# Kernel tuning notes

Measured on AMD Instinct MI355X. Metric: run time of the kernel, lower is better.

Reference implementation:

```python
import jax, jax.numpy as jnp
from jax import lax
import numpy as np

B, C, H, W = 8, 192, 128, 128
HEADS, WS, SS = 6, 8, 4
HID = 768  # 4 * C
HEAD_DIM = C // HEADS
SCALE = HEAD_DIM ** -0.5
EPS = 1e-5


def _rel_pos_index(ws):
    coords = np.stack(np.meshgrid(np.arange(ws), np.arange(ws), indexing='ij'))  # (2, ws, ws)
    flat = coords.reshape(2, ws * ws)
    rel = flat[:, :, None] - flat[:, None, :]          # (2, N, N)
    rel = rel.transpose(1, 2, 0)                       # (N, N, 2)
    rel[:, :, 0] += ws - 1
    rel[:, :, 1] += ws - 1
    rel[:, :, 0] *= 2 * ws - 1
    return rel.sum(-1).astype(np.int32)                # (N, N)


def _attn_mask(hp, wp, ws, ss):
    # Swin shift mask: 0 where tokens share a region, -100 otherwise. (nW, N, N)
    img = np.zeros((hp, wp), dtype=np.float32)
    slices = (slice(0, -ws), slice(-ws, -ss), slice(-ss, None))
    cnt = 0
    for hs in slices:
        for ws_ in slices:
            img[hs, ws_] = float(cnt)
            cnt += 1
    mw = img.reshape(hp // ws, ws, wp // ws, ws).transpose(0, 2, 1, 3).reshape(-1, ws * ws)
    am = mw[:, None, :] - mw[:, :, None]
    return np.where(am != 0, -100.0, 0.0).astype(np.float32)


def _layernorm(x, g, b):
    mu = jnp.mean(x, axis=-1, keepdims=True)
    var = jnp.mean(jnp.square(x - mu), axis=-1, keepdims=True)
    return (x - mu) * lax.rsqrt(var + EPS) * g + b


def setup_inputs() -> dict:
    key = jax.random.key(0)
    ks = jax.random.split(key, 16)
    s = 0.02
    return {
        'x': jax.random.normal(ks[0], (B, C, H, W), jnp.float32),
        'pos_conv_w': jax.random.normal(ks[1], (C, 1, 3, 3), jnp.float32) * s,
        'norm1_g': jnp.ones((C,), jnp.float32),
        'norm1_b': jnp.zeros((C,), jnp.float32),
        'qkv_w': jax.random.normal(ks[2], (C, 3 * C), jnp.float32) * s,
        'qkv_b': jnp.zeros((3 * C,), jnp.float32),
        'proj_w': jax.random.normal(ks[3], (C, C), jnp.float32) * s,
        'proj_b': jnp.zeros((C,), jnp.float32),
        'rel_bias_table': jax.random.normal(ks[4], ((2 * WS - 1) ** 2, HEADS), jnp.float32) * s,
        'norm2_g': jnp.ones((C,), jnp.float32),
        'norm2_b': jnp.zeros((C,), jnp.float32),
        'mlp_w1': jax.random.normal(ks[5], (C, HID), jnp.float32) * s,
        'mlp_b1': jnp.zeros((HID,), jnp.float32),
        'mlp_w2': jax.random.normal(ks[6], (HID, C), jnp.float32) * s,
        'mlp_b2': jnp.zeros((C,), jnp.float32),
    }


def reference(x, pos_conv_w, norm1_g, norm1_b, qkv_w, qkv_b, proj_w, proj_b,
              rel_bias_table, norm2_g, norm2_b, mlp_w1, mlp_b1, mlp_w2, mlp_b2):
    b, c, h, w = x.shape
    ws, ss, nh, hd = WS, SS, HEADS, HEAD_DIM
    N = ws * ws

    # depthwise 3x3 positional conv (residual)
    x = x + lax.conv_general_dilated(
        x, pos_conv_w, (1, 1), 'SAME', feature_group_count=c,
        dimension_numbers=('NCHW', 'OIHW', 'NCHW'))

    if ss > 0:
        x = jnp.roll(x, (-ss, -ss), axis=(2, 3))

    pad_h = (ws - h % ws) % ws
    pad_w = (ws - w % ws) % ws
    if pad_h or pad_w:
        x = jnp.pad(x, ((0, 0), (0, 0), (0, pad_h), (0, pad_w)))
    hp, wp = h + pad_h, w + pad_w

    # window partition -> (num_windows, N, c)
    windows = x.reshape(b, c, hp // ws, ws, wp // ws, ws)
    windows = windows.transpose(0, 2, 4, 3, 5, 1).reshape(-1, N, c)
    nw = windows.shape[0]

    a = _layernorm(windows, norm1_g, norm1_b)
    qkv = (a @ qkv_w + qkv_b).reshape(nw, N, 3, nh, hd).transpose(2, 0, 3, 1, 4)
    q, k, v = qkv[0], qkv[1], qkv[2]                      # (nw, nh, N, hd)

    attn = jnp.einsum('whnd,whmd->whnm', q * SCALE, k)    # (nw, nh, N, N)

    rel_idx = jnp.asarray(_rel_pos_index(ws))             # (N, N) int
    bias = rel_bias_table[rel_idx.reshape(-1)].reshape(N, N, nh).transpose(2, 0, 1)
    attn = attn + bias[None]

    if ss > 0:
        mask = jnp.asarray(_attn_mask(hp, wp, ws, ss))    # (nW_per_img, N, N)
        nwpb = (hp // ws) * (wp // ws)
        attn = attn.reshape(b, nwpb, nh, N, N) + mask[None, :, None]
        attn = attn.reshape(nw, nh, N, N)

    attn = jax.nn.softmax(attn, axis=-1)
    out = jnp.einsum('whnm,whmd->whnd', attn, v).transpose(0, 2, 1, 3).reshape(nw, N, c)

    windows = windows + out @ proj_w + proj_b
    hmid = jax.nn.gelu(_layernorm(windows, norm2_g, norm2_b) @ mlp_w1 + mlp_b1, approximate=False)
    windows = windows + hmid @ mlp_w2 + mlp_b2

    # unpartition -> (b, c, hp, wp), crop, roll back
    y = windows.reshape(b, hp // ws, wp // ws, ws, ws, c)
    y = y.transpose(0, 5, 1, 3, 2, 4).reshape(b, c, hp, wp)[:, :, :h, :w]
    if ss > 0:
        y = jnp.roll(y, (ss, ss), axis=(2, 3))
    return y
```

## Files before the change

### kernel.cpp

```cpp
#include <hip/hip_runtime.h>
#include <hip/hip_bf16.h>
#include <cstdint>
#include <cstddef>

typedef short short8 __attribute__((ext_vector_type(8)));
typedef float float4_ __attribute__((ext_vector_type(4)));
typedef unsigned int uint4_ __attribute__((ext_vector_type(4)));
typedef unsigned int uint2_ __attribute__((ext_vector_type(2)));

#define DEVI static __device__ __forceinline__

DEVI unsigned short f2bf(float f) {
  union { float f; unsigned u; } v; v.f = f;
  return (unsigned short)((v.u + 0x7FFFu + ((v.u >> 16) & 1u)) >> 16);
}
DEVI unsigned pack2bf(float a, float b) {
  return (unsigned)f2bf(a) | ((unsigned)f2bf(b) << 16);
}
DEVI unsigned short f2bfc(float f) {
  __hip_bfloat16 h = __float2bfloat16(f);
  union { __hip_bfloat16 h1; unsigned short u; } cv; cv.h1 = h; return cv.u;
}
DEVI unsigned pack2bfc(float a, float b) {
  float2 f2; f2.x = a; f2.y = b;
  __hip_bfloat162 h = __float22bfloat162_rn(f2);
  union { __hip_bfloat162 h2; unsigned u; } cv; cv.h2 = h; return cv.u;
}
DEVI float bf2f(unsigned short h) {
  union { unsigned u; float f; } v; v.u = ((unsigned)h) << 16;
  return v.f;
}
DEVI float gelu_f(float x) {
  float u = x * (0.7978845608f + 0.0356774081f * x * x);
  float e = exp2f(-2.8853900818f * u);
  return x * __builtin_amdgcn_rcpf(1.0f + e);
}

#define SCALE_Q 0.17677669529663687f

__global__ __launch_bounds__(256) void k_prep(
    const float* __restrict__ qkv_w, const float* __restrict__ qkv_b,
    const float* __restrict__ proj_w, const float* __restrict__ mlp_w1,
    const float* __restrict__ mlp_w2, const float* __restrict__ relt,
    unsigned short* __restrict__ qkvWT, unsigned short* __restrict__ projWT,
    unsigned short* __restrict__ w1T, unsigned short* __restrict__ w2T,
    float* __restrict__ qkv_b_s, float* __restrict__ bias_attn) {
  int i = blockIdx.x * 256 + threadIdx.x;
  if (i < 110592) { int n = i / 192, k = i - n * 192;
    float v = qkv_w[k * 576 + n]; if (n < 192) v *= SCALE_Q;
    qkvWT[i] = f2bf(v); return; }
  i -= 110592;
  if (i < 576) { qkv_b_s[i] = qkv_b[i] * (i < 192 ? SCALE_Q : 1.0f); return; }
  i -= 576;
  if (i < 36864) { int n = i / 192, k = i - n * 192;
    projWT[i] = f2bf(proj_w[k * 192 + n]); return; }
  i -= 36864;
  if (i < 147456) { int n = i / 192, k = i - n * 192;
    w1T[i] = f2bf(mlp_w1[k * 768 + n]); return; }
  i -= 147456;
  if (i < 147456) { int n = i / 768, k = i - n * 768;
    w2T[i] = f2bf(mlp_w2[k * 192 + n]); return; }
  i -= 147456;
  if (i < 24576) {
    int h = i >> 12, nm = i & 4095, n = nm >> 6, m = nm & 63;
    int dr = (n >> 3) - (m >> 3) + 7, dc = (n & 7) - (m & 7) + 7;
    bias_attn[i] = relt[(dr * 15 + dc) * 6 + h];
  }
}

__global__ __launch_bounds__(256) void k_conv(
    const float* __restrict__ x, const float* __restrict__ convw,
    unsigned short* __restrict__ temp) {
  __shared__ float s_in[66 * 128];
  int bx = blockIdx.x;
  int c = bx >> 1, seg = bx & 1, b = blockIdx.y;
  int h0 = seg * 64;
  int t = threadIdx.x;
  const float* xp = x + ((size_t)(b * 192 + c)) * 16384;
  #pragma unroll
  for (int i = 0; i < 9; ++i) {
    int q = t + i * 256;
    if (q < 2112) {
      int srow = q >> 5, chunk = q & 31;
      float4_ v = *(const float4_*)(xp + ((h0 + 3 + srow) & 127) * 128 + chunk * 4);
      *(float4_*)(s_in + srow * 128 + chunk * 4) = v;
    }
  }
  float cw9[9];
  #pragma unroll
  for (int i = 0; i < 9; ++i) cw9[i] = convw[c * 9 + i];
  __syncthreads();
  int r2 = t >> 7;
  int wp = t & 127;
  int w_true = (wp + 4) & 127;
  float mw0 = (w_true != 0) ? 1.f : 0.f;
  float mw2 = (w_true != 127) ? 1.f : 0.f;
  int wl0 = (w_true + 127) & 127, wl2 = (w_true + 1) & 127;
  unsigned short* tp = temp + ((size_t)(b * 192 + c)) * 16384;
  #pragma unroll 4
  for (int it = 0; it < 32; ++it) {
    int r = it * 2 + r2;
    int h_true = (h0 + 4 + r) & 127;
    float mh0 = (h_true != 0) ? 1.f : 0.f;
    float mh2 = (h_true != 127) ? 1.f : 0.f;
    const float* row0 = s_in + r * 128;
    const float* row1 = row0 + 128;
    const float* row2 = row1 + 128;
    float acc = row1[w_true];
    acc = fmaf(cw9[0], mh0 * mw0 * row0[wl0], acc);
    acc = fmaf(cw9[1], mh0 * row0[w_true], acc);
    acc = fmaf(cw9[2], mh0 * mw2 * row0[wl2], acc);
    acc = fmaf(cw9[3], mw0 * row1[wl0], acc);
    acc = fmaf(cw9[4], row1[w_true], acc);
    acc = fmaf(cw9[5], mw2 * row1[wl2], acc);
    acc = fmaf(cw9[6], mh2 * mw0 * row2[wl0], acc);
    acc = fmaf(cw9[7], mh2 * row2[w_true], acc);
    acc = fmaf(cw9[8], mh2 * mw2 * row2[wl2], acc);
    tp[(size_t)(h0 + r) * 128 + wp] = f2bf(acc);
  }
}

__global__ __launch_bounds__(256) void k_lnw(
    const unsigned short* __restrict__ temp, const float* __restrict__ g1,
    const float* __restrict__ b1, unsigned short* __restrict__ xw,
    unsigned short* __restrict__ a) {
  __shared__ unsigned short sT[192 * 128];
  __shared__ float s_g[192], s_b[192];
  int t = threadIdx.x;
  for (int i = t; i < 192; i += 256) { s_g[i] = g1[i]; s_b[i] = b1[i]; }
  int wj0 = blockIdx.x * 2, wi = blockIdx.y, b = blockIdx.z;
  const unsigned short* tb = temp + (size_t)b * (192 * 16384) + (wi * 8) * 128 + wj0 * 8;
  #pragma unroll
  for (int i = 0; i < 12; ++i) {
    int id = t + i * 256;
    int c = id >> 4, rem = id & 15, r = rem >> 1, piece = rem & 1;
    short8 v = *(const short8*)(tb + (size_t)c * 16384 + r * 128 + piece * 8);
    *(short8*)(sT + c * 128 + piece * 64 + r * 8) = v;
  }
  __syncthreads();
  int tok = t >> 1, half = t & 1, c0 = half * 96;
  size_t gtok = ((size_t)(b * 256 + wi * 16 + wj0 + (tok >> 6))) * 64 + (tok & 63);
  unsigned short* xwp = xw + gtok * 192 + c0;
  float sum = 0.f, sq = 0.f;
  #pragma unroll
  for (int j8 = 0; j8 < 12; ++j8) {
    unsigned short raw[8];
    unsigned pk[4];
    #pragma unroll
    for (int e = 0; e < 8; ++e) {
      unsigned short rv = sT[(c0 + j8 * 8 + e) * 128 + tok];
      raw[e] = rv;
      float x = bf2f(rv);
      sum += x; sq = fmaf(x, x, sq);
    }
    #pragma unroll
    for (int k = 0; k < 4; ++k) pk[k] = (unsigned)raw[2 * k] | ((unsigned)raw[2 * k + 1] << 16);
    uint4_ pv = { pk[0], pk[1], pk[2], pk[3] };
    *(uint4_*)(xwp + j8 * 8) = pv;
  }
  sum += __shfl_xor(sum, 1);
  sq  += __shfl_xor(sq, 1);
  float mu = sum * (1.f / 192.f);
  float var = sq * (1.f / 192.f) - mu * mu;
  float rs = rsqrtf(var + 1e-5f);
  unsigned short* ap = a + gtok * 192 + c0;
  #pragma unroll
  for (int j8 = 0; j8 < 12; ++j8) {
    unsigned pk[4];
    #pragma unroll
    for (int k = 0; k < 4; ++k) {
      int c = c0 + j8 * 8 + k * 2;
      float v0 = (bf2f(sT[c * 128 + tok]) - mu) * rs * s_g[c] + s_b[c];
      float v1 = (bf2f(sT[(c + 1) * 128 + tok]) - mu) * rs * s_g[c + 1] + s_b[c + 1];
      pk[k] = pack2bf(v0, v1);
    }
    uint4_ pv = { pk[0], pk[1], pk[2], pk[3] };
    *(uint4_*)(ap + j8 * 8) = pv;
  }
}

__global__ __launch_bounds__(64, 2) void k_qkvattn(
    const unsigned short* __restrict__ a, const unsigned short* __restrict__ wT,
    const float* __restrict__ qbias, const float* __restrict__ biasAll,
    unsigned short* __restrict__ outO) {
  __shared__ __align__(16) unsigned short sQK[4096];
  __shared__ __align__(16) unsigned short sVT[2048];
  int lane = threadIdx.x;
  int head = blockIdx.y;
  int win = blockIdx.x;
  int wi = (win >> 4) & 15, wj = win & 15;
  int lrow = lane & 15, lkgrp = lane >> 4, lk = lkgrp * 8;
  const unsigned short* aWin = a + (size_t)win * (64 * 192);
  const unsigned short* wbase = wT + (size_t)head * 32 * 192;
  char* qk = (char*)sQK;
  char* vt = (char*)sVT;

  float4_ acc[3][2][4];
  #pragma unroll
  for (int s = 0; s < 3; ++s)
    #pragma unroll
    for (int nb = 0; nb < 2; ++nb)
      #pragma unroll
      for (int mi = 0; mi < 4; ++mi) acc[s][nb][mi] = (float4_){0.f, 0.f, 0.f, 0.f};
  short8 bwA[6], bwB[6], af0[4], af1[4];
  #pragma unroll
  for (int s = 0; s < 3; ++s)
    #pragma unroll
    for (int nb = 0; nb < 2; ++nb)
      bwA[s * 2 + nb] = *(const short8*)(wbase + (size_t)(s * 192 + nb * 16 + lrow) * 192 + lk);
  #pragma unroll
  for (int mi = 0; mi < 4; ++mi)
    af0[mi] = *(const short8*)(aWin + (size_t)(mi * 16 + lrow) * 192 + lk);
  #pragma unroll
  for (int s = 0; s < 3; ++s)
    #pragma unroll
    for (int nb = 0; nb < 2; ++nb)
      bwB[s * 2 + nb] = *(const short8*)(wbase + (size_t)(s * 192 + nb * 16 + lrow) * 192 + 32 + lk);
  #pragma unroll
  for (int mi = 0; mi < 4; ++mi)
    af1[mi] = *(const short8*)(aWin + (size_t)(mi * 16 + lrow) * 192 + 32 + lk);
  #pragma unroll
  for (int ks = 0; ks < 6; ++ks) {
    #pragma unroll
    for (int mi = 0; mi < 4; ++mi) {
      short8 a_ = (ks & 1) ? af1[mi] : af0[mi];
      #pragma unroll
      for (int sn = 0; sn < 6; ++sn) {
        short8 b_ = (ks & 1) ? bwB[sn] : bwA[sn];
        acc[sn >> 1][sn & 1][mi] =
            __builtin_amdgcn_mfma_f32_16x16x32_bf16(b_, a_, acc[sn >> 1][sn & 1][mi], 0, 0, 0);
      }
    }
    if (ks < 4) {
      int kc = (ks + 2) * 32 + lk;
      #pragma unroll
      for (int s = 0; s < 3; ++s)
        #pragma unroll
        for (int nb = 0; nb < 2; ++nb) {
          short8 nv = *(const short8*)(wbase + (size_t)(s * 192 + nb * 16 + lrow) * 192 + kc);
          if (ks & 1) bwB[s * 2 + nb] = nv; else bwA[s * 2 + nb] = nv;
        }
      #pragma unroll
      for (int mi = 0; mi < 4; ++mi) {
        short8 nv = *(const short8*)(aWin + (size_t)(mi * 16 + lrow) * 192 + kc);
        if (ks & 1) af1[mi] = nv; else af0[mi] = nv;
      }
    }
  }
  #pragma unroll
  for (int sel = 0; sel < 2; ++sel) {
    #pragma unroll
    for (int nb = 0; nb < 2; ++nb) {
      float4_ b4 = *(const float4_*)(qbias + sel * 192 + head * 32 + nb * 16 + lkgrp * 4);
      int dsub2 = (nb * 16 + lkgrp * 4) * 2;
      #pragma unroll
      for (int mi = 0; mi < 4; ++mi) {
        int tok = mi * 16 + lrow;
        uint2_ pv = { pack2bfc(acc[sel][nb][mi][0] + b4[0], acc[sel][nb][mi][1] + b4[1]),
                      pack2bfc(acc[sel][nb][mi][2] + b4[2], acc[sel][nb][mi][3] + b4[3]) };
        *(uint2_*)(qk + sel * 4096 + ((tok * 64 + dsub2) ^ ((tok & 7) << 4))) = pv;
      }
    }
  }
  #pragma unroll
  for (int nb = 0; nb < 2; ++nb) {
    float4_ b4 = *(const float4_*)(qbias + 384 + head * 32 + nb * 16 + lkgrp * 4);
    #pragma unroll
    for (int mi = 0; mi < 4; ++mi) {
      int tok = mi * 16 + lrow;
      #pragma unroll
      for (int e = 0; e < 4; ++e) {
        int d = nb * 16 + lkgrp * 4 + e;
        *(unsigned short*)(vt + ((d * 128 + tok * 2) ^ ((d & 7) << 4))) =
            f2bfc(acc[2][nb][mi][e] + b4[e]);
      }
    }
  }

  short8 kf[4];
  #pragma unroll
  for (int ni = 0; ni < 4; ++ni) {
    int tokk = ni * 16 + lrow;
    kf[ni] = *(const short8*)(qk + 4096 + ((tokk * 64 + lk * 2) ^ ((tokk & 7) << 4)));
  }
  float4_ s[4][4];
  __builtin_amdgcn_s_setprio(1);
  #pragma unroll
  for (int mi = 0; mi < 4; ++mi) {
    int tokq = mi * 16 + lrow;
    short8 qf = *(const short8*)(qk + ((tokq * 64 + lk * 2) ^ ((tokq & 7) << 4)));
    #pragma unroll
    for (int ni = 0; ni < 4; ++ni) {
      s[mi][ni] = (float4_){0.f, 0.f, 0.f, 0.f};
      s[mi][ni] = __builtin_amdgcn_mfma_f32_16x16x32_bf16(qf, kf[ni], s[mi][ni], 0, 0, 0);
    }
  }
  __builtin_amdgcn_s_setprio(0);
  const float* bh = biasAll + head * 4096;
  bool wi15 = (wi == 15), wj15 = (wj == 15);
  bool edge = wi15 || wj15;
  #pragma unroll
  for (int mi = 0; mi < 4; ++mi) {
    #pragma unroll
    for (int e = 0; e < 4; ++e) {
      int row = mi * 16 + lkgrp * 4 + e;
      int rcls = (wi15 ? ((row >> 3) >= 4 ? 2 : 1) : 0) * 3 +
                 (wj15 ? ((row & 7) >= 4 ? 2 : 1) : 0);
      float v[4];
      #pragma unroll
      for (int ni = 0; ni < 4; ++ni) {
        int col = ni * 16 + lrow;
        float xv = s[mi][ni][e] + bh[row * 64 + col];
        if (edge) {
          int ccls = (wi15 ? ((col >> 3) >= 4 ? 2 : 1) : 0) * 3 +
                     (wj15 ? ((col & 7) >= 4 ? 2 : 1) : 0);
          if (ccls != rcls) xv -= 100.f;
        }
        v[ni] = xv;
      }
      float mx = fmaxf(fmaxf(v[0], v[1]), fmaxf(v[2], v[3]));
      mx = fmaxf(mx, __shfl_xor(mx, 1));
      mx = fmaxf(mx, __shfl_xor(mx, 2));
      mx = fmaxf(mx, __shfl_xor(mx, 4));
      mx = fmaxf(mx, __shfl_xor(mx, 8));
      float sm = 0.f;
      #pragma unroll
      for (int ni = 0; ni < 4; ++ni) { v[ni] = __expf(v[ni] - mx); sm += v[ni]; }
      sm += __shfl_xor(sm, 1);
      sm += __shfl_xor(sm, 2);
      sm += __shfl_xor(sm, 4);
      sm += __shfl_xor(sm, 8);
      float inv = 1.f / sm;
      #pragma unroll
      for (int ni = 0; ni < 4; ++ni) {
        int col = ni * 16 + lrow;
        *(unsigned short*)(qk + ((row * 128 + col * 2) ^ ((row & 7) << 4))) = f2bfc(v[ni] * inv);
      }
    }
  }
  float4_ o[2][4];
  #pragma unroll
  for (int db = 0; db < 2; ++db)
    #pragma unroll
    for (int qb2 = 0; qb2 < 4; ++qb2) o[db][qb2] = (float4_){0.f, 0.f, 0.f, 0.f};
  __builtin_amdgcn_s_setprio(1);
  #pragma unroll
  for (int kk = 0; kk < 2; ++kk) {
    int ktok = kk * 32 + lk;
    short8 vf[2], pf[4];
    #pragma unroll
    for (int db = 0; db < 2; ++db) {
      int d = db * 16 + lrow;
      vf[db] = *(const short8*)(vt + ((d * 128 + ktok * 2) ^ ((d & 7) << 4)));
    }
    #pragma unroll
    for (int qb2 = 0; qb2 < 4; ++qb2) {
      int rq = qb2 * 16 + lrow;
      pf[qb2] = *(const short8*)(qk + ((rq * 128 + ktok * 2) ^ ((rq & 7) << 4)));
    }
    #pragma unroll
    for (int db = 0; db < 2; ++db)
      #pragma unroll
      for (int qb2 = 0; qb2 < 4; ++qb2)
        o[db][qb2] = __builtin_amdgcn_mfma_f32_16x16x32_bf16(vf[db], pf[qb2], o[db][qb2], 0, 0, 0);
  }
  __builtin_amdgcn_s_setprio(0);
  unsigned short* ob = outO + (size_t)win * (64 * 192);
  #pragma unroll
  for (int qb2 = 0; qb2 < 4; ++qb2)
    #pragma unroll
    for (int db = 0; db < 2; ++db) {
      unsigned lo = pack2bfc(o[db][qb2][0], o[db][qb2][1]);
      unsigned hi = pack2bfc(o[db][qb2][2], o[db][qb2][3]);
      uint2_ pv = { lo, hi };
      *(uint2_*)(ob + (size_t)(qb2 * 16 + lrow) * 192 + head * 32 + db * 16 + lkgrp * 4) = pv;
    }
}

__global__ __launch_bounds__(256, 2) void k_mlp(
    const unsigned short* __restrict__ O, const unsigned short* __restrict__ xw,
    const unsigned short* __restrict__ projWT, const float* __restrict__ proj_b,
    const float* __restrict__ n2g, const float* __restrict__ n2b,
    const unsigned short* __restrict__ w1T, const float* __restrict__ mlpb1,
    const unsigned short* __restrict__ w2T, const float* __restrict__ mlpb2,
    float* __restrict__ y) {
  __shared__ __align__(16) unsigned short sH[64 * 192];
  __shared__ __align__(16) unsigned short sB2[64 * 192];
  __shared__ float sRed[64 * 8];
  __shared__ unsigned sTok[64];
  int t = threadIdx.x, lane = t & 63, wn = t >> 6;
  int lrow = lane & 15, lkgrp = lane >> 4, lk = lkgrp * 8;
  int blk = blockIdx.x;
  int b = blk >> 8, rem = blk & 255, ta = rem >> 3, tb_ = rem & 7;
  if (t < 64) {
    int rr = t >> 4, ss = t & 15;
    int h = ta * 4 + rr, w = tb_ * 16 + ss;
    int hp = (h + 124) & 127, wp = (w + 124) & 127;
    unsigned gtok = ((unsigned)(b * 256 + (hp >> 3) * 16 + (wp >> 3))) * 64 +
                    (hp & 7) * 8 + (wp & 7);
    sTok[t] = gtok * 192u;
  }
  __syncthreads();
  unsigned aoff[4];
  #pragma unroll
  for (int mi = 0; mi < 4; ++mi) aoff[mi] = sTok[mi * 16 + lrow];
  float4_ tacc[4][3];
  #pragma unroll
  for (int mi = 0; mi < 4; ++mi)
    #pragma unroll
    for (int ni = 0; ni < 3; ++ni) tacc[mi][ni] = (float4_){0.f, 0.f, 0.f, 0.f};
  {
    short8 bP0[3][3], bP1[3][3], af0[4], af1[4];
    #pragma unroll
    for (int ni = 0; ni < 3; ++ni)
      #pragma unroll
      for (int k3 = 0; k3 < 3; ++k3)
        bP0[ni][k3] = *(const short8*)(projWT + (size_t)(wn * 48 + ni * 16 + lrow) * 192 + k3 * 32 + lk);
    #pragma unroll
    for (int mi = 0; mi < 4; ++mi)
      af0[mi] = *(const short8*)(O + aoff[mi] + lk);
    #pragma unroll
    for (int ni = 0; ni < 3; ++ni)
      #pragma unroll
      for (int k3 = 0; k3 < 3; ++k3)
        bP1[ni][k3] = *(const short8*)(projWT + (size_t)(wn * 48 + ni * 16 + lrow) * 192 + (3 + k3) * 32 + lk);
    #pragma unroll
    for (int mi = 0; mi < 4; ++mi)
      af1[mi] = *(const short8*)(O + aoff[mi] + 32 + lk);
    #pragma unroll
    for (int ks = 0; ks < 6; ++ks) {
      #pragma unroll
      for (int mi = 0; mi < 4; ++mi) {
        short8 a_ = (ks & 1) ? af1[mi] : af0[mi];
        #pragma unroll
        for (int ni = 0; ni < 3; ++ni) {
          short8 b_ = (ks < 3) ? bP0[ni][ks] : bP1[ni][ks - 3];
          tacc[mi][ni] = __builtin_amdgcn_mfma_f32_16x16x32_bf16(a_, b_, tacc[mi][ni], 0, 0, 0);
        }
      }
      if (ks < 4) {
        #pragma unroll
        for (int mi = 0; mi < 4; ++mi) {
          short8 nv = *(const short8*)(O + aoff[mi] + (ks + 2) * 32 + lk);
          if (ks & 1) af1[mi] = nv; else af0[mi] = nv;
        }
      }
    }
  }
  {
    unsigned roff[4][4];
    #pragma unroll
    for (int mi = 0; mi < 4; ++mi)
      #pragma unroll
      for (int e = 0; e < 4; ++e)
        roff[mi][e] = sTok[mi * 16 + lkgrp * 4 + e];
    unsigned short rxv[3][4][4];
    #pragma unroll
    for (int ni = 0; ni < 3; ++ni) {
      int col = wn * 48 + ni * 16 + lrow;
      #pragma unroll
      for (int mi = 0; mi < 4; ++mi)
        #pragma unroll
        for (int e = 0; e < 4; ++e)
          rxv[ni][mi][e] = xw[roff[mi][e] + col];
    }
    #pragma unroll
    for (int ni = 0; ni < 3; ++ni) {
      float pbv = proj_b[wn * 48 + ni * 16 + lrow];
      #pragma unroll
      for (int mi = 0; mi < 4; ++mi)
        #pragma unroll
        for (int e = 0; e < 4; ++e)
          tacc[mi][ni][e] += pbv + bf2f(rxv[ni][mi][e]);
    }
  }
  #pragma unroll
  for (int mi = 0; mi < 4; ++mi)
    #pragma unroll
    for (int e = 0; e < 4; ++e) {
      float s1 = tacc[mi][0][e] + tacc[mi][1][e] + tacc[mi][2][e];
      float s2 = tacc[mi][0][e] * tacc[mi][0][e] + tacc[mi][1][e] * tacc[mi][1][e] +
                 tacc[mi][2][e] * tacc[mi][2][e];
      s1 += __shfl_xor(s1, 1); s1 += __shfl_xor(s1, 2); s1 += __shfl_xor(s1, 4); s1 += __shfl_xor(s1, 8);
      s2 += __shfl_xor(s2, 1); s2 += __shfl_xor(s2, 2); s2 += __shfl_xor(s2, 4); s2 += __shfl_xor(s2, 8);
      if (lrow == 0) {
        int row = mi * 16 + lkgrp * 4 + e;
        sRed[row * 8 + wn * 2 + 0] = s1;
        sRed[row * 8 + wn * 2 + 1] = s2;
      }
    }
  __syncthreads();
  #pragma unroll
  for (int mi = 0; mi < 4; ++mi)
    #pragma unroll
    for (int e = 0; e < 4; ++e) {
      int row = mi * 16 + lkgrp * 4 + e;
      float s1 = sRed[row * 8] + sRed[row * 8 + 2] + sRed[row * 8 + 4] + sRed[row * 8 + 6];
      float s2 = sRed[row * 8 + 1] + sRed[row * 8 + 3] + sRed[row * 8 + 5] + sRed[row * 8 + 7];
      float mu = s1 * (1.f / 192.f);
      float var = s2 * (1.f / 192.f) - mu * mu;
      float rs = rsqrtf(var + 1e-5f);
      #pragma unroll
      for (int ni = 0; ni < 3; ++ni) {
        int col = wn * 48 + ni * 16 + lrow;
        float hv = (tacc[mi][ni][e] - mu) * rs * n2g[col] + n2b[col];
        *(unsigned short*)((char*)sH + ((row * 384 + col * 2) ^ ((row & 7) << 4))) = f2bfc(hv);
      }
    }
  __syncthreads();
  short8 bwA[6], bwB[6];
  #pragma unroll
  for (int ks = 0; ks < 6; ++ks)
    bwA[ks] = *(const short8*)(w1T + (size_t)(wn * 48 + lrow) * 192 + ks * 32 + lk);
  #pragma unroll 1
  for (int ch = 0; ch < 4; ++ch) {
    #pragma unroll 1
    for (int ni = 0; ni < 3; ++ni) {
      int nni = (ni < 2) ? ni + 1 : 0;
      int nch = (ni < 2) ? ch : ch + 1;
      if (nch < 4) {
        int gn = nch * 192 + wn * 48 + nni * 16 + lrow;
        #pragma unroll
        for (int ks = 0; ks < 6; ++ks)
          bwB[ks] = *(const short8*)(w1T + (size_t)gn * 192 + ks * 32 + lk);
      }
      float4_ h1[4];
      #pragma unroll
      for (int mi = 0; mi < 4; ++mi) h1[mi] = (float4_){0.f, 0.f, 0.f, 0.f};
      __builtin_amdgcn_s_setprio(1);
      #pragma unroll
      for (int ks = 0; ks < 6; ++ks) {
        int kb = ks * 32 + lk;
        #pragma unroll
        for (int mi = 0; mi < 4; ++mi) {
          int row = mi * 16 + lrow;
          short8 afv = *(const short8*)((const char*)sH + ((row * 384 + kb * 2) ^ ((row & 7) << 4)));
          h1[mi] = __builtin_amdgcn_mfma_f32_16x16x32_bf16(bwA[ks], afv, h1[mi], 0, 0, 0);
        }
      }
      __builtin_amdgcn_s_setprio(0);
      float4_ b4 = *(const float4_*)(mlpb1 + ch * 192 + wn * 48 + ni * 16 + lkgrp * 4);
      int nsub2 = (wn * 48 + ni * 16 + lkgrp * 4) * 2;
      #pragma unroll
      for (int mi = 0; mi < 4; ++mi) {
        int tok_ = mi * 16 + lrow;
        float g0 = gelu_f(h1[mi][0] + b4[0]);
        float g1 = gelu_f(h1[mi][1] + b4[1]);
        float g2 = gelu_f(h1[mi][2] + b4[2]);
        float g3 = gelu_f(h1[mi][3] + b4[3]);
        uint2_ pv = { pack2bfc(g0, g1), pack2bfc(g2, g3) };
        *(uint2_*)((char*)sB2 + ((tok_ * 384 + nsub2) ^ ((tok_ & 7) << 4))) = pv;
      }
      #pragma unroll
      for (int ks = 0; ks < 6; ++ks) bwA[ks] = bwB[ks];
    }
    short8 cw0[3][3], cw1[3][3];
    #pragma unroll
    for (int ni = 0; ni < 3; ++ni)
      #pragma unroll
      for (int k3 = 0; k3 < 3; ++k3)
        cw0[ni][k3] = *(const short8*)(w2T + (size_t)(wn * 48 + ni * 16 + lrow) * 768 + ch * 192 + k3 * 32 + lk);
    __syncthreads();
    #pragma unroll
    for (int ni = 0; ni < 3; ++ni)
      #pragma unroll
      for (int k3 = 0; k3 < 3; ++k3)
        cw1[ni][k3] = *(const short8*)(w2T + (size_t)(wn * 48 + ni * 16 + lrow) * 768 + ch * 192 + (3 + k3) * 32 + lk);
    __builtin_amdgcn_s_setprio(1);
    #pragma unroll
    for (int ks = 0; ks < 6; ++ks) {
      int kb = ks * 32 + lk;
      short8 af[4];
      #pragma unroll
      for (int mi = 0; mi < 4; ++mi) {
        int row = mi * 16 + lrow;
        af[mi] = *(const short8*)((const char*)sB2 + ((row * 384 + kb * 2) ^ ((row & 7) << 4)));
      }
      #pragma unroll
      for (int mi = 0; mi < 4; ++mi)
        #pragma unroll
        for (int ni = 0; ni < 3; ++ni) {
          short8 b_ = (ks < 3) ? cw0[ni][ks] : cw1[ni][ks - 3];
          tacc[mi][ni] = __builtin_amdgcn_mfma_f32_16x16x32_bf16(af[mi], b_, tacc[mi][ni], 0, 0, 0);
        }
    }
    __builtin_amdgcn_s_setprio(0);
    __syncthreads();
  }
  int wcol = tb_ * 16 + lkgrp * 4;
  #pragma unroll
  for (int ni = 0; ni < 3; ++ni) {
    int col = wn * 48 + ni * 16 + lrow;
    float b2v = mlpb2[col];
    #pragma unroll
    for (int mi = 0; mi < 4; ++mi) {
      int h = ta * 4 + mi;
      float4_ vv;
      #pragma unroll
      for (int e = 0; e < 4; ++e) vv[e] = tacc[mi][ni][e] + b2v;
      *(float4_*)(y + ((size_t)(b * 192 + col) * 128 + h) * 128 + wcol) = vv;
    }
  }
}

extern "C" void kernel_launch(void* const* d_in, const int* in_sizes, int n_in,
                              void* d_out, int out_size, void* d_ws, size_t ws_size,
                              hipStream_t stream) {
  (void)in_sizes; (void)n_in; (void)out_size;
  const float* x    = (const float*)d_in[0];
  const float* pcw  = (const float*)d_in[1];
  const float* n1g  = (const float*)d_in[2];
  const float* n1b  = (const float*)d_in[3];
  const float* qkvw = (const float*)d_in[4];
  const float* qkvb = (const float*)d_in[5];
  const float* pw   = (const float*)d_in[6];
  const float* pb   = (const float*)d_in[7];
  const float* relt = (const float*)d_in[8];
  const float* n2g  = (const float*)d_in[9];
  const float* n2b  = (const float*)d_in[10];
  const float* w1   = (const float*)d_in[11];
  const float* mb1  = (const float*)d_in[12];
  const float* w2   = (const float*)d_in[13];
  const float* mb2  = (const float*)d_in[14];
  float* y = (float*)d_out;
  char* ws = (char*)d_ws;
  size_t off = 0;
  auto carve = [&](size_t bytes) { void* p = ws + off; off += (bytes + 255) & ~(size_t)255; return p; };
  unsigned short* qkvWT  = (unsigned short*)carve(576 * 192 * 2);
  unsigned short* projWT = (unsigned short*)carve(192 * 192 * 2);
  unsigned short* w1T    = (unsigned short*)carve(768 * 192 * 2);
  unsigned short* w2T    = (unsigned short*)carve(192 * 768 * 2);
  float* qkv_b_s   = (float*)carve(576 * 4);
  float* bias_attn = (float*)carve(6 * 64 * 64 * 4);
  unsigned short* aBuf   = (unsigned short*)carve((size_t)131072 * 192 * 2);
  unsigned short* xwBuf  = (unsigned short*)carve((size_t)131072 * 192 * 2);
  unsigned short* temp   = (unsigned short*)carve((size_t)131072 * 192 * 2);
  if (off > ws_size) return;

  k_prep<<<dim3(1827), dim3(256), 0, stream>>>(qkvw, qkvb, pw, w1, w2, relt,
                                               qkvWT, projWT, w1T, w2T, qkv_b_s, bias_attn);
  k_conv<<<dim3(384, 8), dim3(256), 0, stream>>>(x, pcw, temp);
  k_lnw<<<dim3(8, 16, 8), dim3(256), 0, stream>>>(temp, n1g, n1b, xwBuf, aBuf);
  k_qkvattn<<<dim3(2048, 6), dim3(64), 0, stream>>>(aBuf, qkvWT, qkv_b_s, bias_attn, temp);
  k_mlp<<<dim3(2048), dim3(256), 0, stream>>>(temp, xwBuf, projWT, pb, n2g, n2b,
                                              w1T, mb1, w2T, mb2, y);
}
```

Measured before the change: 496.7 us.

## Merge attention heads into one block and double-buffer MLP hidden chunks

The QKV+attention kernel now runs one 384-thread block per window, with one wave per head and per-head shared buffers, instead of one 64-thread block per (window, head). This lets the six heads share the window's activation reads through cache and cuts the block count. In the MLP kernel, the first GEMM now computes all three 16-column tiles per chunk at once with k-step weight streaming. The GELU output alternates between two shared buffers so the trailing per-chunk barrier can be dropped, and the next chunk's weights are prefetched during the second GEMM. The cost is more registers for the h1 accumulators, more shared memory, and possibly lower occupancy.

```diff
diff --git a/kernel.cpp b/kernel.cpp
--- a/kernel.cpp
+++ b/kernel.cpp
@@ -179,21 +179,20 @@
   }
 }
 
-__global__ __launch_bounds__(64, 2) void k_qkvattn(
+__global__ __launch_bounds__(384, 1) void k_qkvattn(
     const unsigned short* __restrict__ a, const unsigned short* __restrict__ wT,
     const float* __restrict__ qbias, const float* __restrict__ biasAll,
     unsigned short* __restrict__ outO) {
-  __shared__ __align__(16) unsigned short sQK[4096];
-  __shared__ __align__(16) unsigned short sVT[2048];
-  int lane = threadIdx.x;
-  int head = blockIdx.y;
+  __shared__ __align__(16) unsigned short sQK[6][4096];
+  __shared__ __align__(16) unsigned short sVT[6][2048];
+  int t = threadIdx.x, lane = t & 63, head = t / 64;
   int win = blockIdx.x;
   int wi = (win >> 4) & 15, wj = win & 15;
   int lrow = lane & 15, lkgrp = lane >> 4, lk = lkgrp * 8;
   const unsigned short* aWin = a + (size_t)win * (64 * 192);
   const unsigned short* wbase = wT + (size_t)head * 32 * 192;
-  char* qk = (char*)sQK;
-  char* vt = (char*)sVT;
+  char* qk = (char*)sQK[head];
+  char* vt = (char*)sVT[head];
 
   float4_ acc[3][2][4];
   #pragma unroll
@@ -204,18 +203,14 @@
       for (int mi = 0; mi < 4; ++mi) acc[s][nb][mi] = (float4_){0.f, 0.f, 0.f, 0.f};
   short8 bwA[6], bwB[6], af0[4], af1[4];
   #pragma unroll
-  for (int s = 0; s < 3; ++s)
-    #pragma unroll
-    for (int nb = 0; nb < 2; ++nb)
-      bwA[s * 2 + nb] = *(const short8*)(wbase + (size_t)(s * 192 + nb * 16 + lrow) * 192 + lk);
+  for (int sn = 0; sn < 6; ++sn)
+    bwA[sn] = *(const short8*)(wbase + (size_t)((sn >> 1) * 192 + (sn & 1) * 16 + lrow) * 192 + lk);
   #pragma unroll
   for (int mi = 0; mi < 4; ++mi)
     af0[mi] = *(const short8*)(aWin + (size_t)(mi * 16 + lrow) * 192 + lk);
   #pragma unroll
-  for (int s = 0; s < 3; ++s)
-    #pragma unroll
-    for (int nb = 0; nb < 2; ++nb)
-      bwB[s * 2 + nb] = *(const short8*)(wbase + (size_t)(s * 192 + nb * 16 + lrow) * 192 + 32 + lk);
+  for (int sn = 0; sn < 6; ++sn)
+    bwB[sn] = *(const short8*)(wbase + (size_t)((sn >> 1) * 192 + (sn & 1) * 16 + lrow) * 192 + 32 + lk);
   #pragma unroll
   for (int mi = 0; mi < 4; ++mi)
     af1[mi] = *(const short8*)(aWin + (size_t)(mi * 16 + lrow) * 192 + 32 + lk);
@@ -234,12 +229,10 @@
     if (ks < 4) {
       int kc = (ks + 2) * 32 + lk;
       #pragma unroll
-      for (int s = 0; s < 3; ++s)
-        #pragma unroll
-        for (int nb = 0; nb < 2; ++nb) {
-          short8 nv = *(const short8*)(wbase + (size_t)(s * 192 + nb * 16 + lrow) * 192 + kc);
-          if (ks & 1) bwB[s * 2 + nb] = nv; else bwA[s * 2 + nb] = nv;
-        }
+      for (int sn = 0; sn < 6; ++sn) {
+        short8 nv = *(const short8*)(wbase + (size_t)((sn >> 1) * 192 + (sn & 1) * 16 + lrow) * 192 + kc);
+        if (ks & 1) bwB[sn] = nv; else bwA[sn] = nv;
+      }
       #pragma unroll
       for (int mi = 0; mi < 4; ++mi) {
         short8 nv = *(const short8*)(aWin + (size_t)(mi * 16 + lrow) * 192 + kc);
@@ -385,7 +378,7 @@
     const unsigned short* __restrict__ w2T, const float* __restrict__ mlpb2,
     float* __restrict__ y) {
   __shared__ __align__(16) unsigned short sH[64 * 192];
-  __shared__ __align__(16) unsigned short sB2[64 * 192];
+  __shared__ __align__(16) unsigned short sB2[2][64 * 192];
   __shared__ float sRed[64 * 8];
   __shared__ unsigned sTok[64];
   int t = threadIdx.x, lane = t & 63, wn = t >> 6;
@@ -508,51 +501,59 @@
       }
     }
   __syncthreads();
-  short8 bwA[6], bwB[6];
-  #pragma unroll
-  for (int ks = 0; ks < 6; ++ks)
-    bwA[ks] = *(const short8*)(w1T + (size_t)(wn * 48 + lrow) * 192 + ks * 32 + lk);
+  short8 wA[3], wB[3];
+  #pragma unroll
+  for (int ni = 0; ni < 3; ++ni)
+    wA[ni] = *(const short8*)(w1T + (size_t)(wn * 48 + ni * 16 + lrow) * 192 + lk);
+  #pragma unroll
+  for (int ni = 0; ni < 3; ++ni)
+    wB[ni] = *(const short8*)(w1T + (size_t)(wn * 48 + ni * 16 + lrow) * 192 + 32 + lk);
   #pragma unroll 1
   for (int ch = 0; ch < 4; ++ch) {
-    #pragma unroll 1
+    char* sBc = (char*)sB2[ch & 1];
+    float4_ h1[4][3];
+    #pragma unroll
+    for (int mi = 0; mi < 4; ++mi)
+      #pragma unroll
+      for (int ni = 0; ni < 3; ++ni) h1[mi][ni] = (float4_){0.f, 0.f, 0.f, 0.f};
+    __builtin_amdgcn_s_setprio(1);
+    #pragma unroll
+    for (int ks = 0; ks < 6; ++ks) {
+      int kb = ks * 32 + lk;
+      #pragma unroll
+      for (int mi = 0; mi < 4; ++mi) {
+        int row = mi * 16 + lrow;
+        short8 afv = *(const short8*)((const char*)sH + ((row * 384 + kb * 2) ^ ((row & 7) << 4)));
+        #pragma unroll
+        for (int ni = 0; ni < 3; ++ni) {
+          short8 b_ = (ks & 1) ? wB[ni] : wA[ni];
+          h1[mi][ni] = __builtin_amdgcn_mfma_f32_16x16x32_bf16(b_, afv, h1[mi][ni], 0, 0, 0);
+        }
+      }
+      if (ks < 4) {
+        int kc = (ks + 2) * 32 + lk;
+        #pragma unroll
+        for (int ni = 0; ni < 3; ++ni) {
+          short8 nv = *(const short8*)(w1T + (size_t)(ch * 192 + wn * 48 + ni * 16 + lrow) * 192 + kc);
+          if (ks & 1) wB[ni] = nv; else wA[ni] = nv;
+        }
+      }
+    }
+    __builtin_amdgcn_s_setprio(0);
+    #pragma unroll
     for (int ni = 0; ni < 3; ++ni) {
-      int nni = (ni < 2) ? ni + 1 : 0;
-      int nch = (ni < 2) ? ch : ch + 1;
-      if (nch < 4) {
-        int gn = nch * 192 + wn * 48 + nni * 16 + lrow;
-        #pragma unroll
-        for (int ks = 0; ks < 6; ++ks)
-          bwB[ks] = *(const short8*)(w1T + (size_t)gn * 192 + ks * 32 + lk);
-      }
-      float4_ h1[4];
-      #pragma unroll
-      for (int mi = 0; mi < 4; ++mi) h1[mi] = (float4_){0.f, 0.f, 0.f, 0.f};
-      __builtin_amdgcn_s_setprio(1);
-      #pragma unroll
-      for (int ks = 0; ks < 6; ++ks) {
-        int kb = ks * 32 + lk;
-        #pragma unroll
-        for (int mi = 0; mi < 4; ++mi) {
-          int row = mi * 16 + lrow;
-          short8 afv = *(const short8*)((const char*)sH + ((row * 384 + kb * 2) ^ ((row & 7) << 4)));
-          h1[mi] = __builtin_amdgcn_mfma_f32_16x16x32_bf16(bwA[ks], afv, h1[mi], 0, 0, 0);
-        }
-      }
-      __builtin_amdgcn_s_setprio(0);
       float4_ b4 = *(const float4_*)(mlpb1 + ch * 192 + wn * 48 + ni * 16 + lkgrp * 4);
       int nsub2 = (wn * 48 + ni * 16 + lkgrp * 4) * 2;
       #pragma unroll
       for (int mi = 0; mi < 4; ++mi) {
         int tok_ = mi * 16 + lrow;
-        float g0 = gelu_f(h1[mi][0] + b4[0]);
-        float g1 = gelu_f(h1[mi][1] + b4[1]);
-        float g2 = gelu_f(h1[mi][2] + b4[2]);
-        float g3 = gelu_f(h1[mi][3] + b4[3]);
+        float g0 = gelu_f(h1[mi][ni][0] + b4[0]);
+        float g1 = gelu_f(h1[mi][ni][1] + b4[1]);
+        float g2 = gelu_f(h1[mi][ni][2] + b4[2]);
+        float g3 = gelu_f(h1[mi][ni][3] + b4[3]);
         uint2_ pv = { pack2bfc(g0, g1), pack2bfc(g2, g3) };
-        *(uint2_*)((char*)sB2 + ((tok_ * 384 + nsub2) ^ ((tok_ & 7) << 4))) = pv;
-      }
-      #pragma unroll
-      for (int ks = 0; ks < 6; ++ks) bwA[ks] = bwB[ks];
+        *(uint2_*)(sBc + ((tok_ * 384 + nsub2) ^ ((tok_ & 7) << 4))) = pv;
+      }
     }
     short8 cw0[3][3], cw1[3][3];
     #pragma unroll
@@ -566,6 +567,15 @@
       #pragma unroll
       for (int k3 = 0; k3 < 3; ++k3)
         cw1[ni][k3] = *(const short8*)(w2T + (size_t)(wn * 48 + ni * 16 + lrow) * 768 + ch * 192 + (3 + k3) * 32 + lk);
+    if (ch < 3) {
+      int gb = (ch + 1) * 192 + wn * 48;
+      #pragma unroll
+      for (int ni = 0; ni < 3; ++ni)
+        wA[ni] = *(const short8*)(w1T + (size_t)(gb + ni * 16 + lrow) * 192 + lk);
+      #pragma unroll
+      for (int ni = 0; ni < 3; ++ni)
+        wB[ni] = *(const short8*)(w1T + (size_t)(gb + ni * 16 + lrow) * 192 + 32 + lk);
+    }
     __builtin_amdgcn_s_setprio(1);
     #pragma unroll
     for (int ks = 0; ks < 6; ++ks) {
@@ -574,7 +584,7 @@
       #pragma unroll
       for (int mi = 0; mi < 4; ++mi) {
         int row = mi * 16 + lrow;
-        af[mi] = *(const short8*)((const char*)sB2 + ((row * 384 + kb * 2) ^ ((row & 7) << 4)));
+        af[mi] = *(const short8*)(sBc + ((row * 384 + kb * 2) ^ ((row & 7) << 4)));
       }
       #pragma unroll
       for (int mi = 0; mi < 4; ++mi)
@@ -585,7 +595,6 @@
         }
     }
     __builtin_amdgcn_s_setprio(0);
-    __syncthreads();
   }
   int wcol = tb_ * 16 + lkgrp * 4;
   #pragma unroll
@@ -641,7 +650,7 @@
                                                qkvWT, projWT, w1T, w2T, qkv_b_s, bias_attn);
   k_conv<<<dim3(384, 8), dim3(256), 0, stream>>>(x, pcw, temp);
   k_lnw<<<dim3(8, 16, 8), dim3(256), 0, stream>>>(temp, n1g, n1b, xwBuf, aBuf);
-  k_qkvattn<<<dim3(2048, 6), dim3(64), 0, stream>>>(aBuf, qkvWT, qkv_b_s, bias_attn, temp);
+  k_qkvattn<<<dim3(2048), dim3(384), 0, stream>>>(aBuf, qkvWT, qkv_b_s, bias_attn, temp);
   k_mlp<<<dim3(2048), dim3(256), 0, stream>>>(temp, xwBuf, projWT, pb, n2g, n2b,
                                               w1T, mb1, w2T, mb2, y);
 }
```

After: 484.1 us, median of 2. 1.03x faster.
